# Performance work log

Hardware: AMD Instinct MI355X
Metric: run time of the kernel (lower is better)

The kernel has to match this reference:

```python
import jax, jax.numpy as jnp
import numpy as np

MEM_SLOTS, NUM_HEADS, HEAD_SIZE, KEY_SIZE = 8, 8, 128, 128
MEM_SIZE = NUM_HEADS * HEAD_SIZE  # 1024
NUM_GATES = 2 * MEM_SIZE          # 2048 (gate_style='unit')
B, T, INPUT_SIZE = 128, 32, 1024


def _ln(x, g, b, eps=1e-5):
    m = x.mean(-1, keepdims=True)
    v = ((x - m) ** 2).mean(-1, keepdims=True)
    return (x - m) / jnp.sqrt(v + eps) * g + b


def setup_inputs() -> dict:
    key = jax.random.key(0)
    ks = jax.random.split(key, 12)
    s = 0.02  # weight init scale
    memory = jnp.tile(jnp.eye(MEM_SLOTS, MEM_SIZE, dtype=jnp.float32)[None], (B, 1, 1))
    return {
        'x': jax.random.normal(ks[0], (B, T, INPUT_SIZE), jnp.float32),
        'memory': memory,
        'Wi': s * jax.random.normal(ks[1], (INPUT_SIZE, MEM_SIZE), jnp.float32),
        'bi': jnp.zeros((MEM_SIZE,), jnp.float32),
        'Wq': s * jax.random.normal(ks[2], (MEM_SIZE, KEY_SIZE * NUM_HEADS), jnp.float32),
        'bq': jnp.zeros((KEY_SIZE * NUM_HEADS,), jnp.float32),
        'Wk': s * jax.random.normal(ks[3], (MEM_SIZE, KEY_SIZE * NUM_HEADS), jnp.float32),
        'bk': jnp.zeros((KEY_SIZE * NUM_HEADS,), jnp.float32),
        'Wv': s * jax.random.normal(ks[4], (MEM_SIZE, HEAD_SIZE * NUM_HEADS), jnp.float32),
        'bv': jnp.zeros((HEAD_SIZE * NUM_HEADS,), jnp.float32),
        'Wm': s * jax.random.normal(ks[5], (MEM_SIZE, MEM_SIZE), jnp.float32),
        'bm': jnp.zeros((MEM_SIZE,), jnp.float32),
        'ln1_g': jnp.ones((MEM_SIZE,), jnp.float32),
        'ln1_b': jnp.zeros((MEM_SIZE,), jnp.float32),
        'ln2_g': jnp.ones((MEM_SIZE,), jnp.float32),
        'ln2_b': jnp.zeros((MEM_SIZE,), jnp.float32),
        'rep_w': jax.random.normal(ks[6], (MEM_SIZE,), jnp.float32),
        'Wg': s * jax.random.normal(ks[7], (MEM_SIZE, NUM_GATES), jnp.float32),
        'bg': jnp.zeros((NUM_GATES,), jnp.float32),
        'Wmg': 0.01 * jax.random.normal(ks[8], (MEM_SLOTS, MEM_SIZE, NUM_GATES), jnp.float32),
        'forget_bias': jnp.asarray(1.0, jnp.float32),
        'input_bias': jnp.asarray(0.0, jnp.float32),
    }


def reference(x, memory, Wi, bi, Wq, bq, Wk, bk, Wv, bv, Wm, bm,
              ln1_g, ln1_b, ln2_g, ln2_b, rep_w, Wg, bg, Wmg,
              forget_bias, input_bias):
    Bx, S, D, H, K = x.shape[0], MEM_SLOTS, MEM_SIZE, NUM_HEADS, KEY_SIZE

    def step(mem, xt):                             # mem: (B,S,D), xt: (B,input)
        inp = xt @ Wi + bi                         # input_projector -> (B,D)
        inp_r = inp[:, None, :]                    # (B,1,D)
        # --- multihead attention: q from memory, k/v from projected input ---
        q = (mem @ Wq + bq).reshape(Bx, S, H, K).transpose(0, 2, 1, 3)   # (B,H,S,K)
        k = (inp_r @ Wk + bk).reshape(Bx, 1, H, K).transpose(0, 2, 1, 3)  # (B,H,1,K)
        v = (inp_r @ Wv + bv).reshape(Bx, 1, H, HEAD_SIZE).transpose(0, 2, 1, 3)
        scores = jax.nn.softmax(jnp.einsum('bhsk,bhtk->bhst', q, k), axis=-1)  # unscaled, per source
        att = jnp.einsum('bhst,bhtd->bhsd', scores, v)
        att = att.transpose(0, 2, 1, 3).reshape(Bx, S, D)
        # --- residual + LN, shared-weight 2-layer relu MLP, residual + LN ---
        m1 = _ln(mem + att, ln1_g, ln1_b)
        h = jax.nn.relu(m1 @ Wm + bm)
        h = jax.nn.relu(h @ Wm + bm)               # ModuleList([l]*2) shares weights
        m2 = _ln(m1 + h, ln2_g, ln2_b)
        # --- gates (computed from OLD memory and projected input) ---
        gi = (jax.nn.relu(rep_w * inp_r).mean(axis=1) @ Wg + bg)[:, None, :]  # RepeatLinear
        gm = jnp.einsum('bsd,sdg->bsg', jnp.tanh(mem), Wmg)                    # GroupLinearLayer
        gates = gm + gi                                                        # (B,S,2D)
        ig, fg = jnp.split(gates, 2, axis=-1)
        ig = jax.nn.sigmoid(ig + input_bias)
        fg = jax.nn.sigmoid(fg + forget_bias)
        new_mem = ig * jnp.tanh(m2) + fg * mem
        return new_mem, new_mem.reshape(Bx, S * D)

    final_mem, outs = jax.lax.scan(step, memory, x.transpose(1, 0, 2))
    return outs, final_mem  # outs: (T,B,S*D)
```

## Files before the change

kernel.cpp:

```cpp
#include <hip/hip_runtime.h>
#include <math.h>

#define DMEM   1024
#define NGATES 2048
#define NB     128
#define NT     32

__device__ inline float sigm(float x) { return 1.f / (1.f + __expf(-x)); }

template<int AMODE>
__global__ __launch_bounds__(256)
void gemm128(const float* __restrict__ A, int lda,
             const float* __restrict__ rep,
             const float* __restrict__ W, int N,
             const float* __restrict__ bias,
             float* __restrict__ C, int K)
{
    __shared__ float As[16][132];
    __shared__ float Bs[16][132];
    const int tid  = threadIdx.x;
    const int tr   = (tid >> 4) << 2;
    const int tc   = (tid & 15) << 2;
    const int row0 = blockIdx.y * 128, col0 = blockIdx.x * 128;
    const int arow = tid >> 1, ah = (tid & 1) * 8;
    const int brow = tid >> 4, bcol = (tid & 15) * 8;

    float4 a0, a1, b0, b1;
    auto LOAD = [&](int k0) {
        const float* ap = A + (long)(row0 + arow) * lda + k0 + ah;
        a0 = *(const float4*)ap;
        a1 = *(const float4*)(ap + 4);
        if (AMODE == 2) {
            float4 r0 = *(const float4*)(rep + k0 + ah);
            float4 r1 = *(const float4*)(rep + k0 + ah + 4);
            a0.x = fmaxf(a0.x * r0.x, 0.f); a0.y = fmaxf(a0.y * r0.y, 0.f);
            a0.z = fmaxf(a0.z * r0.z, 0.f); a0.w = fmaxf(a0.w * r0.w, 0.f);
            a1.x = fmaxf(a1.x * r1.x, 0.f); a1.y = fmaxf(a1.y * r1.y, 0.f);
            a1.z = fmaxf(a1.z * r1.z, 0.f); a1.w = fmaxf(a1.w * r1.w, 0.f);
        }
        const float* bp = W + (long)(k0 + brow) * N + col0 + bcol;
        b0 = *(const float4*)bp;
        b1 = *(const float4*)(bp + 4);
    };

    float acc[8][8] = {};
    LOAD(0);
    const int NIT = K >> 4;
    for (int it = 0; it < NIT; ++it) {
        __syncthreads();
        As[ah + 0][arow] = a0.x; As[ah + 1][arow] = a0.y;
        As[ah + 2][arow] = a0.z; As[ah + 3][arow] = a0.w;
        As[ah + 4][arow] = a1.x; As[ah + 5][arow] = a1.y;
        As[ah + 6][arow] = a1.z; As[ah + 7][arow] = a1.w;
        *(float4*)&Bs[brow][bcol]     = b0;
        *(float4*)&Bs[brow][bcol + 4] = b1;
        __syncthreads();
        if (it + 1 < NIT) LOAD((it + 1) << 4);
#pragma unroll
        for (int kk = 0; kk < 16; ++kk) {
            float a[8], b[8];
            *(float4*)&a[0] = *(const float4*)&As[kk][tr];
            *(float4*)&a[4] = *(const float4*)&As[kk][64 + tr];
            *(float4*)&b[0] = *(const float4*)&Bs[kk][tc];
            *(float4*)&b[4] = *(const float4*)&Bs[kk][64 + tc];
#pragma unroll
            for (int i = 0; i < 8; ++i)
#pragma unroll
                for (int j = 0; j < 8; ++j)
                    acc[i][j] = fmaf(a[i], b[j], acc[i][j]);
        }
    }

#pragma unroll
    for (int jh = 0; jh < 2; ++jh) {
        int cbase = col0 + jh * 64 + tc;
        float4 bv = *(const float4*)&bias[cbase];
#pragma unroll
        for (int ih = 0; ih < 2; ++ih) {
#pragma unroll
            for (int i = 0; i < 4; ++i) {
                int row = row0 + ih * 64 + tr + i;
                *(float4*)(C + (long)row * N + cbase) =
                    make_float4(acc[ih * 4 + i][jh * 4 + 0] + bv.x,
                                acc[ih * 4 + i][jh * 4 + 1] + bv.y,
                                acc[ih * 4 + i][jh * 4 + 2] + bv.z,
                                acc[ih * 4 + i][jh * 4 + 3] + bv.w);
            }
        }
    }
}

template<int AMODE>
__device__ __forceinline__ void gemm64_core(
    const float* __restrict__ A, int lda, long psA,
    const float* __restrict__ abias,
    const float* __restrict__ W, int ldw,
    float* __restrict__ C, int ldc,
    int row0, int col0, int kbeg, int kend,
    float (*As)[68], float (*Bs)[68])
{
    const int tid  = threadIdx.x;
    const int tr   = (tid >> 4) << 2, tc = (tid & 15) << 2;
    const int arow = tid >> 2, aseg = (tid & 3) * 8;
    const int brow = tid >> 3, bcol = (tid & 7) * 8;

    float4 a0, a1, b0, b1;
    auto LOAD = [&](int k0) {
        const float* ap = A + (long)(row0 + arow) * lda + k0 + aseg;
        if (AMODE == 0) {
            a0 = *(const float4*)ap;
            a1 = *(const float4*)(ap + 4);
        } else {
            float4 p0 = *(const float4*)ap;
            float4 p1 = *(const float4*)(ap + psA);
            float4 q0 = *(const float4*)(ap + 4);
            float4 q1 = *(const float4*)(ap + psA + 4);
            float4 c0 = *(const float4*)(abias + k0 + aseg);
            float4 c1 = *(const float4*)(abias + k0 + aseg + 4);
            a0.x = fmaxf(p0.x + p1.x + c0.x, 0.f);
            a0.y = fmaxf(p0.y + p1.y + c0.y, 0.f);
            a0.z = fmaxf(p0.z + p1.z + c0.z, 0.f);
            a0.w = fmaxf(p0.w + p1.w + c0.w, 0.f);
            a1.x = fmaxf(q0.x + q1.x + c1.x, 0.f);
            a1.y = fmaxf(q0.y + q1.y + c1.y, 0.f);
            a1.z = fmaxf(q0.z + q1.z + c1.z, 0.f);
            a1.w = fmaxf(q0.w + q1.w + c1.w, 0.f);
        }
        const float* bp = W + (long)(k0 + brow) * ldw + col0 + bcol;
        b0 = *(const float4*)bp;
        b1 = *(const float4*)(bp + 4);
    };

    float acc[4][4] = {};
    LOAD(kbeg);
    const int NIT = (kend - kbeg) >> 5;
    for (int it = 0; it < NIT; ++it) {
        __syncthreads();
        As[aseg + 0][arow] = a0.x; As[aseg + 1][arow] = a0.y;
        As[aseg + 2][arow] = a0.z; As[aseg + 3][arow] = a0.w;
        As[aseg + 4][arow] = a1.x; As[aseg + 5][arow] = a1.y;
        As[aseg + 6][arow] = a1.z; As[aseg + 7][arow] = a1.w;
        *(float4*)&Bs[brow][bcol]     = b0;
        *(float4*)&Bs[brow][bcol + 4] = b1;
        __syncthreads();
        if (it + 1 < NIT) LOAD(kbeg + ((it + 1) << 5));
#pragma unroll
        for (int kk = 0; kk < 32; ++kk) {
            float4 av = *(const float4*)&As[kk][tr];
            float4 bv = *(const float4*)&Bs[kk][tc];
            acc[0][0] = fmaf(av.x, bv.x, acc[0][0]); acc[0][1] = fmaf(av.x, bv.y, acc[0][1]);
            acc[0][2] = fmaf(av.x, bv.z, acc[0][2]); acc[0][3] = fmaf(av.x, bv.w, acc[0][3]);
            acc[1][0] = fmaf(av.y, bv.x, acc[1][0]); acc[1][1] = fmaf(av.y, bv.y, acc[1][1]);
            acc[1][2] = fmaf(av.y, bv.z, acc[1][2]); acc[1][3] = fmaf(av.y, bv.w, acc[1][3]);
            acc[2][0] = fmaf(av.z, bv.x, acc[2][0]); acc[2][1] = fmaf(av.z, bv.y, acc[2][1]);
            acc[2][2] = fmaf(av.z, bv.z, acc[2][2]); acc[2][3] = fmaf(av.z, bv.w, acc[2][3]);
            acc[3][0] = fmaf(av.w, bv.x, acc[3][0]); acc[3][1] = fmaf(av.w, bv.y, acc[3][1]);
            acc[3][2] = fmaf(av.w, bv.z, acc[3][2]); acc[3][3] = fmaf(av.w, bv.w, acc[3][3]);
        }
    }

#pragma unroll
    for (int i = 0; i < 4; ++i)
        *(float4*)(C + (long)(row0 + tr + i) * ldc + col0 + tc) =
            make_float4(acc[i][0], acc[i][1], acc[i][2], acc[i][3]);
}

template<int LVL>
__global__ __launch_bounds__(256)
void step_gemms(const float* __restrict__ m1, const float* __restrict__ Wm,
                const float* __restrict__ bm,
                float* __restrict__ hP, float* __restrict__ h2P,
                const float* __restrict__ tm, const float* __restrict__ Wmg,
                float* __restrict__ gm)
{
    __shared__ float As[32][68];
    __shared__ float Bs[32][68];
    const int bid = blockIdx.x;
    if (bid < 512) {
        int x = bid & 15, y = (bid >> 4) & 15, kc = bid >> 8;
        if (LVL == 0)
            gemm64_core<0>(m1, 1024, 0, nullptr, Wm, 1024,
                           hP + (long)kc * 1048576, 1024,
                           y * 64, x * 64, kc * 512, kc * 512 + 512, As, Bs);
        else
            gemm64_core<1>(hP, 1024, 1048576, bm, Wm, 1024,
                           h2P + (long)kc * 1048576, 1024,
                           y * 64, x * 64, kc * 512, kc * 512 + 512, As, Bs);
    } else {
        int j = bid - 512;
        int x = (j & 15) + (LVL == 0 ? 0 : 16);
        int y = (j >> 4) & 1, s = j >> 5;
        gemm64_core<0>(tm + s * 1024, 8192, 0, nullptr,
                       Wmg + (long)s * 2097152, 2048,
                       gm + s * 2048, 16384,
                       y * 64, x * 64, 0, 1024, As, Bs);
    }
}

__device__ inline void block_reduce2(float& s1, float& s2)
{
    __shared__ float red[2][4];
    __syncthreads();
#pragma unroll
    for (int off = 32; off > 0; off >>= 1) {
        s1 += __shfl_down(s1, off, 64);
        s2 += __shfl_down(s2, off, 64);
    }
    int tid = threadIdx.x;
    if ((tid & 63) == 0) { red[0][tid >> 6] = s1; red[1][tid >> 6] = s2; }
    __syncthreads();
    s1 = red[0][0] + red[0][1] + red[0][2] + red[0][3];
    s2 = red[1][0] + red[1][1] + red[1][2] + red[1][3];
}

__global__ __launch_bounds__(256)
void ln1_kern(const float* __restrict__ memprev, const float* __restrict__ v,
              const float* __restrict__ g, const float* __restrict__ bb,
              float* __restrict__ m1, float* __restrict__ tm)
{
    const int row = blockIdx.x;
    const int b   = row >> 3;
    const int d   = threadIdx.x << 2;

    float4 mv = *(const float4*)(memprev + (long)row * DMEM + d);
    float4 vv = *(const float4*)(v + ((long)b * NT) * DMEM + d);

    *(float4*)(tm + (long)row * DMEM + d) =
        make_float4(tanhf(mv.x), tanhf(mv.y), tanhf(mv.z), tanhf(mv.w));

    float x0 = mv.x + vv.x, x1 = mv.y + vv.y, x2 = mv.z + vv.z, x3 = mv.w + vv.w;
    float s1 = x0 + x1 + x2 + x3;
    float s2 = x0 * x0 + x1 * x1 + x2 * x2 + x3 * x3;
    block_reduce2(s1, s2);
    float mean = s1 * (1.f / 1024.f);
    float var  = s2 * (1.f / 1024.f) - mean * mean;
    float inv  = 1.f / sqrtf(var + 1e-5f);

    float4 gg = *(const float4*)&g[d];
    float4 bv = *(const float4*)&bb[d];
    *(float4*)(m1 + (long)row * DMEM + d) =
        make_float4((x0 - mean) * inv * gg.x + bv.x,
                    (x1 - mean) * inv * gg.y + bv.y,
                    (x2 - mean) * inv * gg.z + bv.z,
                    (x3 - mean) * inv * gg.w + bv.w);
}

__global__ __launch_bounds__(256)
void step_fused(const float* m1in, const float* __restrict__ h2P,
                const float* __restrict__ bm,
                const float* __restrict__ g2, const float* __restrict__ b2,
                const float* __restrict__ gm, const float* __restrict__ gi, int t,
                const float* __restrict__ memprev,
                const float* __restrict__ fbp, const float* __restrict__ ibp,
                const float* __restrict__ v,
                const float* __restrict__ g1, const float* __restrict__ b1,
                float* __restrict__ outp, float* m1out,
                float* __restrict__ tm, int last)
{
    const int row = blockIdx.x;
    const int b   = row >> 3;
    const int d   = threadIdx.x << 2;
    const long o  = (long)row * DMEM + d;

    float4 a  = *(const float4*)(m1in + o);
    float4 q0 = *(const float4*)(h2P + o);
    float4 q1 = *(const float4*)(h2P + 1048576 + o);
    float4 bb = *(const float4*)&bm[d];
    float x0 = a.x + fmaxf(q0.x + q1.x + bb.x, 0.f);
    float x1 = a.y + fmaxf(q0.y + q1.y + bb.y, 0.f);
    float x2 = a.z + fmaxf(q0.z + q1.z + bb.z, 0.f);
    float x3 = a.w + fmaxf(q0.w + q1.w + bb.w, 0.f);

    float s1 = x0 + x1 + x2 + x3;
    float s2 = x0 * x0 + x1 * x1 + x2 * x2 + x3 * x3;
    block_reduce2(s1, s2);
    float mean = s1 * (1.f / 1024.f);
    float var  = s2 * (1.f / 1024.f) - mean * mean;
    float inv  = 1.f / sqrtf(var + 1e-5f);

    float4 gg = *(const float4*)&g2[d];
    float4 b2v = *(const float4*)&b2[d];
    float t20 = tanhf((x0 - mean) * inv * gg.x + b2v.x);
    float t21 = tanhf((x1 - mean) * inv * gg.y + b2v.y);
    float t22 = tanhf((x2 - mean) * inv * gg.z + b2v.z);
    float t23 = tanhf((x3 - mean) * inv * gg.w + b2v.w);

    const float ib = *ibp, fb = *fbp;
    const long go = (long)row * NGATES + d;
    float4 ge0 = *(const float4*)(gm + go);
    float4 ge1 = *(const float4*)(gm + go + DMEM);
    const long io = ((long)b * NT + t) * NGATES + d;
    float4 i0 = *(const float4*)(gi + io);
    float4 i1 = *(const float4*)(gi + io + DMEM);
    float4 mv = *(const float4*)(memprev + o);

    float4 out;
    out.x = sigm(ge0.x + i0.x + ib) * t20 + sigm(ge1.x + i1.x + fb) * mv.x;
    out.y = sigm(ge0.y + i0.y + ib) * t21 + sigm(ge1.y + i1.y + fb) * mv.y;
    out.z = sigm(ge0.z + i0.z + ib) * t22 + sigm(ge1.z + i1.z + fb) * mv.z;
    out.w = sigm(ge0.w + i0.w + ib) * t23 + sigm(ge1.w + i1.w + fb) * mv.w;
    *(float4*)(outp + o) = out;

    if (!last) {
        float4 vv = *(const float4*)(v + ((long)b * NT + t + 1) * DMEM + d);
        *(float4*)(tm + o) =
            make_float4(tanhf(out.x), tanhf(out.y), tanhf(out.z), tanhf(out.w));

        float y0 = out.x + vv.x, y1 = out.y + vv.y;
        float y2 = out.z + vv.z, y3 = out.w + vv.w;
        float u1 = y0 + y1 + y2 + y3;
        float u2 = y0 * y0 + y1 * y1 + y2 * y2 + y3 * y3;
        block_reduce2(u1, u2);
        float mean1 = u1 * (1.f / 1024.f);
        float var1  = u2 * (1.f / 1024.f) - mean1 * mean1;
        float inv1  = 1.f / sqrtf(var1 + 1e-5f);

        float4 g1v = *(const float4*)&g1[d];
        float4 b1v = *(const float4*)&b1[d];
        *(float4*)(m1out + o) =
            make_float4((y0 - mean1) * inv1 * g1v.x + b1v.x,
                        (y1 - mean1) * inv1 * g1v.y + b1v.y,
                        (y2 - mean1) * inv1 * g1v.z + b1v.z,
                        (y3 - mean1) * inv1 * g1v.w + b1v.w);
    }
}

extern "C" void kernel_launch(void* const* d_in, const int* in_sizes, int n_in,
                              void* d_out, int out_size, void* d_ws, size_t ws_size,
                              hipStream_t stream)
{
    const float* x    = (const float*)d_in[0];
    const float* mem0 = (const float*)d_in[1];
    const float* Wi   = (const float*)d_in[2];
    const float* bi   = (const float*)d_in[3];
    const float* Wv   = (const float*)d_in[8];
    const float* bv   = (const float*)d_in[9];
    const float* Wm   = (const float*)d_in[10];
    const float* bm   = (const float*)d_in[11];
    const float* ln1g = (const float*)d_in[12];
    const float* ln1b = (const float*)d_in[13];
    const float* ln2g = (const float*)d_in[14];
    const float* ln2b = (const float*)d_in[15];
    const float* repw = (const float*)d_in[16];
    const float* Wg   = (const float*)d_in[17];
    const float* bg   = (const float*)d_in[18];
    const float* Wmg  = (const float*)d_in[19];
    const float* fbp  = (const float*)d_in[20];
    const float* ibp  = (const float*)d_in[21];

    float* out = (float*)d_out;
    char*  ws  = (char*)d_ws;
    const long MB = 1024L * 1024L;

    float* v    = (float*)(ws + 0 * MB);
    float* gi   = (float*)(ws + 16 * MB);
    float* m1   = (float*)(ws + 48 * MB);
    float* tm   = (float*)(ws + 52 * MB);
    float* hP   = (float*)(ws + 56 * MB);
    float* gm   = (float*)(ws + 64 * MB);
    float* h2P  = (float*)(ws + 72 * MB);
    float* inp  = (float*)(ws + 48 * MB);

    dim3 blk(256);

    gemm128<0><<<dim3(8, 32, 1), blk, 0, stream>>>(x, 1024, nullptr,
                                                   Wi, 1024, bi, inp, 1024);
    gemm128<0><<<dim3(8, 32, 1), blk, 0, stream>>>(inp, 1024, nullptr,
                                                   Wv, 1024, bv, v, 1024);
    gemm128<2><<<dim3(16, 32, 1), blk, 0, stream>>>(inp, 1024, repw,
                                                    Wg, 2048, bg, gi, 1024);

    ln1_kern<<<1024, blk, 0, stream>>>(mem0, v, ln1g, ln1b, m1, tm);

    const long stepN = (long)NB * 8 * DMEM;
    for (int t = 0; t < NT; ++t) {
        const float* memprev = (t == 0) ? mem0 : out + (long)(t - 1) * stepN;

        step_gemms<0><<<768, blk, 0, stream>>>(m1, Wm, bm, hP, h2P, tm, Wmg, gm);
        step_gemms<1><<<768, blk, 0, stream>>>(m1, Wm, bm, hP, h2P, tm, Wmg, gm);
        step_fused<<<1024, blk, 0, stream>>>(
            m1, h2P, bm, ln2g, ln2b, gm, gi, t, memprev, fbp, ibp,
            v, ln1g, ln1b, out + (long)t * stepN, m1, tm,
            (t == NT - 1) ? 1 : 0);
    }

    hipMemcpyAsync(out + 32L * stepN, out + 31L * stepN, stepN * sizeof(float),
                   hipMemcpyDeviceToDevice, stream);
}
```

Before: 5.279 ms.

## Split-K the input projection, merge v/gate GEMMs, deepen step GEMM K-tile

```diff
diff --git a/kernel.cpp b/kernel.cpp
--- a/kernel.cpp
+++ b/kernel.cpp
@@ -9,19 +9,17 @@
 __device__ inline float sigm(float x) { return 1.f / (1.f + __expf(-x)); }
 
 template<int AMODE>
-__global__ __launch_bounds__(256)
-void gemm128(const float* __restrict__ A, int lda,
-             const float* __restrict__ rep,
-             const float* __restrict__ W, int N,
-             const float* __restrict__ bias,
-             float* __restrict__ C, int K)
-{
-    __shared__ float As[16][132];
-    __shared__ float Bs[16][132];
+__device__ __forceinline__ void gemm128_core(
+    const float* __restrict__ A, int lda, long psA,
+    const float* __restrict__ abias, const float* __restrict__ rep,
+    const float* __restrict__ W, int ldw,
+    const float* __restrict__ bias,
+    float* __restrict__ C, int ldc,
+    int row0, int col0, int kbeg, int kend,
+    float (*As)[132], float (*Bs)[132])
+{
     const int tid  = threadIdx.x;
-    const int tr   = (tid >> 4) << 2;
-    const int tc   = (tid & 15) << 2;
-    const int row0 = blockIdx.y * 128, col0 = blockIdx.x * 128;
+    const int tr   = (tid >> 4) << 2, tc = (tid & 15) << 2;
     const int arow = tid >> 1, ah = (tid & 1) * 8;
     const int brow = tid >> 4, bcol = (tid & 15) * 8;
 
@@ -30,22 +28,32 @@
         const float* ap = A + (long)(row0 + arow) * lda + k0 + ah;
         a0 = *(const float4*)ap;
         a1 = *(const float4*)(ap + 4);
-        if (AMODE == 2) {
-            float4 r0 = *(const float4*)(rep + k0 + ah);
-            float4 r1 = *(const float4*)(rep + k0 + ah + 4);
-            a0.x = fmaxf(a0.x * r0.x, 0.f); a0.y = fmaxf(a0.y * r0.y, 0.f);
-            a0.z = fmaxf(a0.z * r0.z, 0.f); a0.w = fmaxf(a0.w * r0.w, 0.f);
-            a1.x = fmaxf(a1.x * r1.x, 0.f); a1.y = fmaxf(a1.y * r1.y, 0.f);
-            a1.z = fmaxf(a1.z * r1.z, 0.f); a1.w = fmaxf(a1.w * r1.w, 0.f);
-        }
-        const float* bp = W + (long)(k0 + brow) * N + col0 + bcol;
+        if (AMODE >= 1) {
+            float4 p0 = *(const float4*)(ap + psA);
+            float4 p1 = *(const float4*)(ap + psA + 4);
+            float4 c0 = *(const float4*)(abias + k0 + ah);
+            float4 c1 = *(const float4*)(abias + k0 + ah + 4);
+            a0.x += p0.x + c0.x; a0.y += p0.y + c0.y;
+            a0.z += p0.z + c0.z; a0.w += p0.w + c0.w;
+            a1.x += p1.x + c1.x; a1.y += p1.y + c1.y;
+            a1.z += p1.z + c1.z; a1.w += p1.w + c1.w;
+            if (AMODE == 2) {
+                float4 r0 = *(const float4*)(rep + k0 + ah);
+                float4 r1 = *(const float4*)(rep + k0 + ah + 4);
+                a0.x = fmaxf(a0.x * r0.x, 0.f); a0.y = fmaxf(a0.y * r0.y, 0.f);
+                a0.z = fmaxf(a0.z * r0.z, 0.f); a0.w = fmaxf(a0.w * r0.w, 0.f);
+                a1.x = fmaxf(a1.x * r1.x, 0.f); a1.y = fmaxf(a1.y * r1.y, 0.f);
+                a1.z = fmaxf(a1.z * r1.z, 0.f); a1.w = fmaxf(a1.w * r1.w, 0.f);
+            }
+        }
+        const float* bp = W + (long)(k0 + brow) * ldw + col0 + bcol;
         b0 = *(const float4*)bp;
         b1 = *(const float4*)(bp + 4);
     };
 
     float acc[8][8] = {};
-    LOAD(0);
-    const int NIT = K >> 4;
+    LOAD(kbeg);
+    const int NIT = (kend - kbeg) >> 4;
     for (int it = 0; it < NIT; ++it) {
         __syncthreads();
         As[ah + 0][arow] = a0.x; As[ah + 1][arow] = a0.y;
@@ -55,7 +63,7 @@
         *(float4*)&Bs[brow][bcol]     = b0;
         *(float4*)&Bs[brow][bcol + 4] = b1;
         __syncthreads();
-        if (it + 1 < NIT) LOAD((it + 1) << 4);
+        if (it + 1 < NIT) LOAD(kbeg + ((it + 1) << 4));
 #pragma unroll
         for (int kk = 0; kk < 16; ++kk) {
             float a[8], b[8];
@@ -74,19 +82,57 @@
 #pragma unroll
     for (int jh = 0; jh < 2; ++jh) {
         int cbase = col0 + jh * 64 + tc;
-        float4 bv = *(const float4*)&bias[cbase];
+        float4 bv = make_float4(0.f, 0.f, 0.f, 0.f);
+        if (bias) bv = *(const float4*)&bias[cbase];
 #pragma unroll
         for (int ih = 0; ih < 2; ++ih) {
 #pragma unroll
             for (int i = 0; i < 4; ++i) {
                 int row = row0 + ih * 64 + tr + i;
-                *(float4*)(C + (long)row * N + cbase) =
+                *(float4*)(C + (long)row * ldc + cbase) =
                     make_float4(acc[ih * 4 + i][jh * 4 + 0] + bv.x,
                                 acc[ih * 4 + i][jh * 4 + 1] + bv.y,
                                 acc[ih * 4 + i][jh * 4 + 2] + bv.z,
                                 acc[ih * 4 + i][jh * 4 + 3] + bv.w);
             }
         }
+    }
+}
+
+__global__ __launch_bounds__(256, 3)
+void gemm_inp(const float* __restrict__ x, const float* __restrict__ Wi,
+              float* __restrict__ inpP)
+{
+    __shared__ float As[16][132];
+    __shared__ float Bs[16][132];
+    const int bid = blockIdx.x;
+    const int kc = bid >> 8, j = bid & 255;
+    gemm128_core<0>(x, 1024, 0, nullptr, nullptr, Wi, 1024, nullptr,
+                    inpP + (long)kc * 4194304, 1024,
+                    (j >> 3) * 128, (j & 7) * 128, kc * 512, kc * 512 + 512,
+                    As, Bs);
+}
+
+__global__ __launch_bounds__(256, 3)
+void phaseA2(const float* __restrict__ inpP, const float* __restrict__ bi,
+             const float* __restrict__ repw,
+             const float* __restrict__ Wv, const float* __restrict__ bv,
+             float* __restrict__ v,
+             const float* __restrict__ Wg, const float* __restrict__ bg,
+             float* __restrict__ gi)
+{
+    __shared__ float As[16][132];
+    __shared__ float Bs[16][132];
+    const int bid = blockIdx.x;
+    if (bid < 256) {
+        gemm128_core<1>(inpP, 1024, 4194304, bi, nullptr, Wv, 1024, bv,
+                        v, 1024, (bid >> 3) * 128, (bid & 7) * 128, 0, 1024,
+                        As, Bs);
+    } else {
+        int j = bid - 256;
+        gemm128_core<2>(inpP, 1024, 4194304, bi, repw, Wg, 2048, bg,
+                        gi, 2048, (j >> 4) * 128, (j & 15) * 128, 0, 1024,
+                        As, Bs);
     }
 }
 
@@ -101,51 +147,48 @@
 {
     const int tid  = threadIdx.x;
     const int tr   = (tid >> 4) << 2, tc = (tid & 15) << 2;
-    const int arow = tid >> 2, aseg = (tid & 3) * 8;
-    const int brow = tid >> 3, bcol = (tid & 7) * 8;
-
-    float4 a0, a1, b0, b1;
+    const int arow = tid >> 2;
+    const int aseg = (tid & 3) * 16;
+
+    float4 a[4], b[4];
     auto LOAD = [&](int k0) {
         const float* ap = A + (long)(row0 + arow) * lda + k0 + aseg;
-        if (AMODE == 0) {
-            a0 = *(const float4*)ap;
-            a1 = *(const float4*)(ap + 4);
-        } else {
-            float4 p0 = *(const float4*)ap;
-            float4 p1 = *(const float4*)(ap + psA);
-            float4 q0 = *(const float4*)(ap + 4);
-            float4 q1 = *(const float4*)(ap + psA + 4);
-            float4 c0 = *(const float4*)(abias + k0 + aseg);
-            float4 c1 = *(const float4*)(abias + k0 + aseg + 4);
-            a0.x = fmaxf(p0.x + p1.x + c0.x, 0.f);
-            a0.y = fmaxf(p0.y + p1.y + c0.y, 0.f);
-            a0.z = fmaxf(p0.z + p1.z + c0.z, 0.f);
-            a0.w = fmaxf(p0.w + p1.w + c0.w, 0.f);
-            a1.x = fmaxf(q0.x + q1.x + c1.x, 0.f);
-            a1.y = fmaxf(q0.y + q1.y + c1.y, 0.f);
-            a1.z = fmaxf(q0.z + q1.z + c1.z, 0.f);
-            a1.w = fmaxf(q0.w + q1.w + c1.w, 0.f);
-        }
-        const float* bp = W + (long)(k0 + brow) * ldw + col0 + bcol;
-        b0 = *(const float4*)bp;
-        b1 = *(const float4*)(bp + 4);
+#pragma unroll
+        for (int j = 0; j < 4; ++j) {
+            if (AMODE == 0) {
+                a[j] = *(const float4*)(ap + j * 4);
+            } else {
+                float4 p0 = *(const float4*)(ap + j * 4);
+                float4 p1 = *(const float4*)(ap + psA + j * 4);
+                float4 c0 = *(const float4*)(abias + k0 + aseg + j * 4);
+                a[j].x = fmaxf(p0.x + p1.x + c0.x, 0.f);
+                a[j].y = fmaxf(p0.y + p1.y + c0.y, 0.f);
+                a[j].z = fmaxf(p0.z + p1.z + c0.z, 0.f);
+                a[j].w = fmaxf(p0.w + p1.w + c0.w, 0.f);
+            }
+        }
+        const float* bp = W + (long)(k0 + arow) * ldw + col0 + aseg;
+#pragma unroll
+        for (int j = 0; j < 4; ++j) b[j] = *(const float4*)(bp + j * 4);
     };
 
     float acc[4][4] = {};
     LOAD(kbeg);
-    const int NIT = (kend - kbeg) >> 5;
+    const int NIT = (kend - kbeg) >> 6;
     for (int it = 0; it < NIT; ++it) {
         __syncthreads();
-        As[aseg + 0][arow] = a0.x; As[aseg + 1][arow] = a0.y;
-        As[aseg + 2][arow] = a0.z; As[aseg + 3][arow] = a0.w;
-        As[aseg + 4][arow] = a1.x; As[aseg + 5][arow] = a1.y;
-        As[aseg + 6][arow] = a1.z; As[aseg + 7][arow] = a1.w;
-        *(float4*)&Bs[brow][bcol]     = b0;
-        *(float4*)&Bs[brow][bcol + 4] = b1;
+#pragma unroll
+        for (int j = 0; j < 4; ++j) {
+            As[aseg + j * 4 + 0][arow] = a[j].x;
+            As[aseg + j * 4 + 1][arow] = a[j].y;
+            As[aseg + j * 4 + 2][arow] = a[j].z;
+            As[aseg + j * 4 + 3][arow] = a[j].w;
+            *(float4*)&Bs[arow][aseg + j * 4] = b[j];
+        }
         __syncthreads();
-        if (it + 1 < NIT) LOAD(kbeg + ((it + 1) << 5));
-#pragma unroll
-        for (int kk = 0; kk < 32; ++kk) {
+        if (it + 1 < NIT) LOAD(kbeg + ((it + 1) << 6));
+#pragma unroll
+        for (int kk = 0; kk < 64; ++kk) {
             float4 av = *(const float4*)&As[kk][tr];
             float4 bv = *(const float4*)&Bs[kk][tc];
             acc[0][0] = fmaf(av.x, bv.x, acc[0][0]); acc[0][1] = fmaf(av.x, bv.y, acc[0][1]);
@@ -166,15 +209,15 @@
 }
 
 template<int LVL>
-__global__ __launch_bounds__(256)
+__global__ __launch_bounds__(256, 3)
 void step_gemms(const float* __restrict__ m1, const float* __restrict__ Wm,
                 const float* __restrict__ bm,
                 float* __restrict__ hP, float* __restrict__ h2P,
                 const float* __restrict__ tm, const float* __restrict__ Wmg,
                 float* __restrict__ gm)
 {
-    __shared__ float As[32][68];
-    __shared__ float Bs[32][68];
+    __shared__ float As[64][68];
+    __shared__ float Bs[64][68];
     const int bid = blockIdx.x;
     if (bid < 512) {
         int x = bid & 15, y = (bid >> 4) & 15, kc = bid >> 8;
@@ -354,21 +397,17 @@
 
     float* v    = (float*)(ws + 0 * MB);
     float* gi   = (float*)(ws + 16 * MB);
+    float* inpP = (float*)(ws + 48 * MB);
     float* m1   = (float*)(ws + 48 * MB);
     float* tm   = (float*)(ws + 52 * MB);
     float* hP   = (float*)(ws + 56 * MB);
     float* gm   = (float*)(ws + 64 * MB);
     float* h2P  = (float*)(ws + 72 * MB);
-    float* inp  = (float*)(ws + 48 * MB);
 
     dim3 blk(256);
 
-    gemm128<0><<<dim3(8, 32, 1), blk, 0, stream>>>(x, 1024, nullptr,
-                                                   Wi, 1024, bi, inp, 1024);
-    gemm128<0><<<dim3(8, 32, 1), blk, 0, stream>>>(inp, 1024, nullptr,
-                                                   Wv, 1024, bv, v, 1024);
-    gemm128<2><<<dim3(16, 32, 1), blk, 0, stream>>>(inp, 1024, repw,
-                                                    Wg, 2048, bg, gi, 1024);
+    gemm_inp<<<512, blk, 0, stream>>>(x, Wi, inpP);
+    phaseA2<<<768, blk, 0, stream>>>(inpP, bi, repw, Wv, bv, v, Wg, bg, gi);
 
     ln1_kern<<<1024, blk, 0, stream>>>(mem0, v, ln1g, ln1b, m1, tm);
 
```

New measurement: 8.115 ms. 53.7% more time.
